# Performance work log

Hardware: AMD Instinct MI355X
Metric: run time of the kernel (lower is better)

## Reference

```python
import jax, jax.numpy as jnp
import numpy as np

BATCH, NUM_MASKS, IN_DIM, OUT_DIM = 512, 16, 1024, 1024


def setup_inputs() -> dict:
    key = jax.random.key(0)
    k1, k2, k3 = jax.random.split(key, 3)
    x = jax.random.normal(k1, (BATCH, NUM_MASKS, IN_DIM), dtype=jnp.float32)
    kernel = jax.random.normal(k2, (IN_DIM, OUT_DIM), dtype=jnp.float32) * (1.0 / np.sqrt(IN_DIM))
    masks = jax.random.uniform(k3, (NUM_MASKS, IN_DIM, OUT_DIM), dtype=jnp.float32)
    return {"x": x, "kernel": kernel, "masks": masks}


def reference(x, kernel, masks):
    # masked_kernel[m, i, o] = kernel[i, o] * masks[m, i, o]
    masked_kernel = kernel[None, :, :] * masks  # (M, I, O)
    # Original tf.scan serializes batch; equivalent math is one batched einsum:
    # out[b, m, o] = sum_i x[b, m, i] * masked_kernel[m, i, o]
    # NOTE: the executed tf.scan path applies NO activation, so neither do we.
    out = jnp.einsum('bmi,mio->bmo', x, masked_kernel)  # (B, M, O)
    return out
```

## Files before the change

kernel.cpp:

```cpp
#include <hip/hip_runtime.h>
#include <hip/hip_bf16.h>


#define BATCH 512
#define NMASK 16
#define IN_D  1024
#define OUT_D 1024

#define BM 128
#define BN 128
#define BK 32
#define NT (IN_D / BK)
#define AKP 40
#define BKP 36
#define THREADS 512

using bf16x8  = __attribute__((ext_vector_type(8))) __bf16;
using bf16x4t = __attribute__((ext_vector_type(4))) __bf16;
using f32x4   = __attribute__((ext_vector_type(4))) float;
using f32x2   = __attribute__((ext_vector_type(2))) float;
using u16x8   = __attribute__((ext_vector_type(8))) unsigned short;
using u16x4   = __attribute__((ext_vector_type(4))) unsigned short;

__device__ __forceinline__ unsigned short f2bf(float f) {
    unsigned u = __float_as_uint(f);
    u += 0x7fffu + ((u >> 16) & 1u);
    return (unsigned short)(u >> 16);
}

__global__ void __launch_bounds__(THREADS, 4)
mdl_mfma_kernel(const float* __restrict__ X,
                const float* __restrict__ Kn,
                const float* __restrict__ Mk,
                float* __restrict__ Out)
{
    __shared__ __align__(16) unsigned short As[BM * AKP];
    __shared__ __align__(16) unsigned short Bs[BN * BKP];

    const int t = threadIdx.x;
    const int l = t & 63;
    const int w = t >> 6;

    const int raw = blockIdx.x;
    const int wg  = (raw & 7) * 64 + (raw >> 3);
    const int m   = wg >> 5;
    const int ob  = (wg >> 2) & 7;
    const int bb  = wg & 3;

    const int wr = w >> 2;
    const int wc = w & 3;

    f32x4 acc[4][2];
#pragma unroll
    for (int mi = 0; mi < 4; ++mi)
#pragma unroll
        for (int ni = 0; ni < 2; ++ni)
            acc[mi][ni] = (f32x4){0.f, 0.f, 0.f, 0.f};

    const int a_row = t >> 2;
    const int a_k   = (t & 3) * 8;
    const int o_l = (t & 63) * 2;
    const int i_l = (t >> 6) * 4;
    const int ig  = t >> 6;

    const float* Xa  = X + ((size_t)(bb * BM + a_row) * NMASK + m) * IN_D + a_k;
    const float* Knb = Kn + (size_t)i_l * OUT_D + ob * BN + o_l;
    const float* Mkb = Mk + ((size_t)m * IN_D + i_l) * OUT_D + ob * BN + o_l;

    for (int tt = 0; tt < NT; ++tt) {
        const int kt = tt * BK;

        f32x4 av0 = *(const f32x4*)(Xa + kt);
        f32x4 av1 = *(const f32x4*)(Xa + kt + 4);
        f32x2 kv[4], mv[4];
#pragma unroll
        for (int r = 0; r < 4; ++r) {
            kv[r] = *(const f32x2*)(Knb + (size_t)(kt + r) * OUT_D);
            mv[r] = *(const f32x2*)(Mkb + (size_t)(kt + r) * OUT_D);
        }

        __syncthreads();

        {
            u16x8 v;
#pragma unroll
            for (int j = 0; j < 4; ++j) { v[j] = f2bf(av0[j]); v[4 + j] = f2bf(av1[j]); }
            *(u16x8*)(&As[a_row * AKP + a_k]) = v;
        }
#pragma unroll
        for (int c = 0; c < 2; ++c) {
            u16x4 v;
#pragma unroll
            for (int r = 0; r < 4; ++r) v[r] = f2bf(kv[r][c] * mv[r][c]);
            *(u16x4*)(&Bs[(o_l + c) * BKP + ig * 4]) = v;
        }

        __syncthreads();

        const int kg = (l >> 4) * 8;
        bf16x8 af[4], bf[2];
#pragma unroll
        for (int mi = 0; mi < 4; ++mi) {
            const int r = wr * 64 + mi * 16 + (l & 15);
            af[mi] = *(const bf16x8*)(&As[r * AKP + kg]);
        }
#pragma unroll
        for (int ni = 0; ni < 2; ++ni) {
            const int n = wc * 32 + ni * 16 + (l & 15);
            bf16x4t lo = *(const bf16x4t*)(&Bs[n * BKP + kg]);
            bf16x4t hi = *(const bf16x4t*)(&Bs[n * BKP + kg + 4]);
            bf16x8 f;
            f[0] = lo[0]; f[1] = lo[1]; f[2] = lo[2]; f[3] = lo[3];
            f[4] = hi[0]; f[5] = hi[1]; f[6] = hi[2]; f[7] = hi[3];
            bf[ni] = f;
        }
#pragma unroll
        for (int mi = 0; mi < 4; ++mi)
#pragma unroll
            for (int ni = 0; ni < 2; ++ni)
                acc[mi][ni] = __builtin_amdgcn_mfma_f32_16x16x32_bf16(
                    af[mi], bf[ni], acc[mi][ni], 0, 0, 0);
    }

    const int r0 = bb * BM + wr * 64 + (l >> 4) * 4;
    const int c0 = ob * BN + wc * 32 + (l & 15);
#pragma unroll
    for (int mi = 0; mi < 4; ++mi) {
#pragma unroll
        for (int j = 0; j < 4; ++j) {
            const size_t row = (size_t)(r0 + mi * 16 + j);
            float* op = Out + (row * NMASK + m) * OUT_D + c0;
#pragma unroll
            for (int ni = 0; ni < 2; ++ni)
                op[ni * 16] = acc[mi][ni][j];
        }
    }
}

extern "C" void kernel_launch(void* const* d_in, const int* in_sizes, int n_in,
                              void* d_out, int out_size, void* d_ws, size_t ws_size,
                              hipStream_t stream) {
    (void)in_sizes; (void)n_in; (void)d_ws; (void)ws_size; (void)out_size;
    const float* X  = (const float*)d_in[0];
    const float* Kn = (const float*)d_in[1];
    const float* Mk = (const float*)d_in[2];
    float* Out = (float*)d_out;

    const int nblocks = (BATCH / BM) * (OUT_D / BN) * NMASK;
    mdl_mfma_kernel<<<nblocks, THREADS, 0, stream>>>(X, Kn, Mk, Out);
}
```

Baseline: 55.50 us.

## Double-buffer shared tiles and prefetch next K-tile during MFMA

Adds two LDS buffers for the A and B tiles. Global loads for the next K-step are issued before the MFMA phase on the current buffer and stored into the other buffer afterwards, so each iteration needs one barrier instead of two. The B row pitch also changes from 36 to 34 elements, which alters the LDS bank mapping. The cost is roughly double the LDS footprint and higher register pressure from holding prefetched values across the MFMA phase. The 34-element pitch may break the 8-byte alignment of the vector LDS accesses.

```diff
diff --git a/kernel.cpp b/kernel.cpp
--- a/kernel.cpp
+++ b/kernel.cpp
@@ -12,7 +12,7 @@
 #define BK 32
 #define NT (IN_D / BK)
 #define AKP 40
-#define BKP 36
+#define BKP 34
 #define THREADS 512
 
 using bf16x8  = __attribute__((ext_vector_type(8))) __bf16;
@@ -34,8 +34,8 @@
                 const float* __restrict__ Mk,
                 float* __restrict__ Out)
 {
-    __shared__ __align__(16) unsigned short As[BM * AKP];
-    __shared__ __align__(16) unsigned short Bs[BN * BKP];
+    __shared__ __align__(16) unsigned short As[2][BM * AKP];
+    __shared__ __align__(16) unsigned short Bs[2][BN * BKP];
 
     const int t = threadIdx.x;
     const int l = t & 63;
@@ -60,66 +60,79 @@
     const int a_row = t >> 2;
     const int a_k   = (t & 3) * 8;
     const int o_l = (t & 63) * 2;
-    const int i_l = (t >> 6) * 4;
     const int ig  = t >> 6;
+    const int i_l = ig * 4;
 
     const float* Xa  = X + ((size_t)(bb * BM + a_row) * NMASK + m) * IN_D + a_k;
     const float* Knb = Kn + (size_t)i_l * OUT_D + ob * BN + o_l;
     const float* Mkb = Mk + ((size_t)m * IN_D + i_l) * OUT_D + ob * BN + o_l;
 
-    for (int tt = 0; tt < NT; ++tt) {
-        const int kt = tt * BK;
+    f32x4 av0, av1;
+    f32x2 kv[4], mv[4];
 
-        f32x4 av0 = *(const f32x4*)(Xa + kt);
-        f32x4 av1 = *(const f32x4*)(Xa + kt + 4);
-        f32x2 kv[4], mv[4];
+    auto LOAD = [&](int kt) {
+        av0 = *(const f32x4*)(Xa + kt);
+        av1 = *(const f32x4*)(Xa + kt + 4);
 #pragma unroll
         for (int r = 0; r < 4; ++r) {
             kv[r] = *(const f32x2*)(Knb + (size_t)(kt + r) * OUT_D);
             mv[r] = *(const f32x2*)(Mkb + (size_t)(kt + r) * OUT_D);
         }
+    };
 
-        __syncthreads();
-
-        {
-            u16x8 v;
+    auto STORE = [&](int buf) {
+        u16x8 va;
 #pragma unroll
-            for (int j = 0; j < 4; ++j) { v[j] = f2bf(av0[j]); v[4 + j] = f2bf(av1[j]); }
-            *(u16x8*)(&As[a_row * AKP + a_k]) = v;
-        }
+        for (int j = 0; j < 4; ++j) { va[j] = f2bf(av0[j]); va[4 + j] = f2bf(av1[j]); }
+        *(u16x8*)(&As[buf][a_row * AKP + a_k]) = va;
 #pragma unroll
         for (int c = 0; c < 2; ++c) {
             u16x4 v;
 #pragma unroll
             for (int r = 0; r < 4; ++r) v[r] = f2bf(kv[r][c] * mv[r][c]);
-            *(u16x4*)(&Bs[(o_l + c) * BKP + ig * 4]) = v;
+            *(u16x4*)(&Bs[buf][(o_l + c) * BKP + ig * 4]) = v;
         }
+    };
 
-        __syncthreads();
-
+    auto MFMA_PHASE = [&](int buf) {
         const int kg = (l >> 4) * 8;
-        bf16x8 af[4], bf[2];
+        bf16x8 af[4], bfv[2];
 #pragma unroll
         for (int mi = 0; mi < 4; ++mi) {
             const int r = wr * 64 + mi * 16 + (l & 15);
-            af[mi] = *(const bf16x8*)(&As[r * AKP + kg]);
+            af[mi] = *(const bf16x8*)(&As[buf][r * AKP + kg]);
         }
 #pragma unroll
         for (int ni = 0; ni < 2; ++ni) {
             const int n = wc * 32 + ni * 16 + (l & 15);
-            bf16x4t lo = *(const bf16x4t*)(&Bs[n * BKP + kg]);
-            bf16x4t hi = *(const bf16x4t*)(&Bs[n * BKP + kg + 4]);
+            bf16x4t lo = *(const bf16x4t*)(&Bs[buf][n * BKP + kg]);
+            bf16x4t hi = *(const bf16x4t*)(&Bs[buf][n * BKP + kg + 4]);
             bf16x8 f;
             f[0] = lo[0]; f[1] = lo[1]; f[2] = lo[2]; f[3] = lo[3];
             f[4] = hi[0]; f[5] = hi[1]; f[6] = hi[2]; f[7] = hi[3];
-            bf[ni] = f;
+            bfv[ni] = f;
         }
 #pragma unroll
         for (int mi = 0; mi < 4; ++mi)
 #pragma unroll
             for (int ni = 0; ni < 2; ++ni)
                 acc[mi][ni] = __builtin_amdgcn_mfma_f32_16x16x32_bf16(
-                    af[mi], bf[ni], acc[mi][ni], 0, 0, 0);
+                    af[mi], bfv[ni], acc[mi][ni], 0, 0, 0);
+    };
+
+    LOAD(0);
+    STORE(0);
+    __syncthreads();
+    int cur = 0;
+    for (int tt = 0; tt < NT; ++tt) {
+        if (tt + 1 < NT) {
+            LOAD((tt + 1) * BK);
+            __builtin_amdgcn_sched_barrier(0);
+        }
+        MFMA_PHASE(cur);
+        if (tt + 1 < NT) STORE(cur ^ 1);
+        __syncthreads();
+        cur ^= 1;
     }
 
     const int r0 = bb * BM + wr * 64 + (l >> 4) * 4;
```

New measurement: 52.34 us. 5.7% less time.
